# Kernel optimization log

Measured on AMD Instinct MI355X. Metric: run time of the kernel, lower is better.

Reference implementation:

```python
import jax, jax.numpy as jnp
import numpy as np
from itertools import product

B, D, H, W = 2, 32, 256, 256
N = 150000
C_IN, C_MID, C_OUT = 16, 32, 64
STRIDE, PAD, K = 2, 1, 3
DO = (D + 2 * PAD - K) // STRIDE + 1
HO = (H + 2 * PAD - K) // STRIDE + 1
WO = (W + 2 * PAD - K) // STRIDE + 1
EPS = 1e-5


def setup_inputs() -> dict:
    key = jax.random.key(0)
    ks = jax.random.split(key, 8)
    # unique active voxel coords via permutation of linear grid indices
    lin = jax.random.permutation(ks[0], B * D * H * W)[:N]
    b = lin // (D * H * W); r = lin % (D * H * W)
    z = r // (H * W); r = r % (H * W)
    y = r // W; x = r % W
    coords = jnp.stack([b, z, y, x], axis=1).astype(jnp.int32)  # [N,4] = (batch,z,y,x)
    feats = jax.random.normal(ks[1], (N, C_IN), jnp.float32)
    W1 = jax.random.normal(ks[2], (27, C_IN, C_MID), jnp.float32) * 0.08
    W2 = jax.random.normal(ks[3], (27, C_MID, C_MID), jnp.float32) * 0.06
    W3 = jax.random.normal(ks[4], (27, C_MID, C_OUT), jnp.float32) * 0.06
    b1 = jnp.zeros((C_MID,), jnp.float32); g1 = jnp.ones((C_MID,), jnp.float32); be1 = jnp.zeros((C_MID,), jnp.float32)
    b2 = jnp.zeros((C_MID,), jnp.float32); g2 = jnp.ones((C_MID,), jnp.float32); be2 = jnp.zeros((C_MID,), jnp.float32)
    b3 = jnp.zeros((C_OUT,), jnp.float32); g3 = jnp.ones((C_OUT,), jnp.float32); be3 = jnp.zeros((C_OUT,), jnp.float32)
    return dict(feats=feats, coords=coords, W1=W1, b1=b1, g1=g1, be1=be1,
                W2=W2, b2=b2, g2=g2, be2=be2, W3=W3, b3=b3, g3=g3, be3=be3)


def _bn_relu(x, g, b):
    # BatchNorm1d (training batch stats, biased var) over active voxels + ReLU
    m = x.mean(0)
    v = ((x - m) ** 2).mean(0)
    return jax.nn.relu((x - m) * jax.lax.rsqrt(v + EPS) * g + b)


def _subm_conv(feats, coords, grid, Wk, bias):
    # submanifold conv: gather neighbor features per kernel offset, GEMM, accumulate
    bb, zz, yy, xx = coords[:, 0], coords[:, 1], coords[:, 2], coords[:, 3]
    acc = jnp.zeros((feats.shape[0], Wk.shape[-1]), feats.dtype)
    for ki, (dz, dy, dx) in enumerate(product((-1, 0, 1), repeat=3)):
        nz, ny, nx = zz + dz, yy + dy, xx + dx
        valid = (nz >= 0) & (nz < D) & (ny >= 0) & (ny < H) & (nx >= 0) & (nx < W)
        lin = ((bb * D + jnp.clip(nz, 0, D - 1)) * H + jnp.clip(ny, 0, H - 1)) * W + jnp.clip(nx, 0, W - 1)
        nidx = jnp.where(valid, grid[lin], -1)
        gathered = jnp.where((nidx >= 0)[:, None], feats[jnp.maximum(nidx, 0)], 0.0)
        acc = acc + gathered @ Wk[ki]
    return acc + bias


def _sparse_down_conv(feats, coords, Wk, bias):
    # stride-2 SparseConv3d as GEMM + scatter-add into downsampled dense grid; mask = active outputs
    bb, zz, yy, xx = coords[:, 0], coords[:, 1], coords[:, 2], coords[:, 3]
    M = B * DO * HO * WO
    out = jnp.zeros((M, Wk.shape[-1]), feats.dtype)
    cnt = jnp.zeros((M,), jnp.int32)
    for ki, (kz, ky, kx) in enumerate(product(range(K), repeat=3)):
        oz, oy, ox = zz + PAD - kz, yy + PAD - ky, xx + PAD - kx
        valid = ((oz % STRIDE == 0) & (oy % STRIDE == 0) & (ox % STRIDE == 0) &
                 (oz >= 0) & (oy >= 0) & (ox >= 0) &
                 (oz // STRIDE < DO) & (oy // STRIDE < HO) & (ox // STRIDE < WO))
        lin = ((bb * DO + jnp.clip(oz // STRIDE, 0, DO - 1)) * HO
               + jnp.clip(oy // STRIDE, 0, HO - 1)) * WO + jnp.clip(ox // STRIDE, 0, WO - 1)
        lin = jnp.where(valid, lin, 0)
        contrib = jnp.where(valid[:, None], feats @ Wk[ki], 0.0)
        out = out.at[lin].add(contrib)
        cnt = cnt.at[lin].add(valid.astype(jnp.int32))
    mask = cnt > 0
    out = jnp.where(mask[:, None], out + bias, 0.0)
    return out, mask


def reference(feats, coords, W1, b1, g1, be1, W2, b2, g2, be2, W3, b3, g3, be3):
    lin0 = ((coords[:, 0] * D + coords[:, 1]) * H + coords[:, 2]) * W + coords[:, 3]
    grid = jnp.full((B * D * H * W,), -1, jnp.int32).at[lin0].set(jnp.arange(N, dtype=jnp.int32))
    x = _bn_relu(_subm_conv(feats, coords, grid, W1, b1), g1, be1)
    x = _bn_relu(_subm_conv(x, coords, grid, W2, b2), g2, be2)
    out, mask = _sparse_down_conv(x, coords, W3, b3)
    nact = jnp.maximum(mask.sum(), 1).astype(out.dtype)
    m = out.sum(0) / nact  # inactive rows are zero
    v = jnp.where(mask[:, None], (out - m) ** 2, 0.0).sum(0) / nact
    out = jax.nn.relu((out - m) * jax.lax.rsqrt(v + EPS) * g3 + be3)
    out = jnp.where(mask[:, None], out, 0.0)
    return out.reshape(B, DO, HO, WO, C_OUT)
```

## Files before the change

### kernel.cpp

```cpp
#include <hip/hip_runtime.h>

#define B_   2
#define D_   32
#define H_   256
#define W_   256
#define N_   150000
#define CIN  16
#define CMID 32
#define COUT 64
#define DO_  16
#define HO_  128
#define WO_  128
#define M_   (B_*DO_*HO_*WO_)
#define EPSf 1e-5f
#define NB_DOWN 8192
#define NREP 64

typedef _Float16 h2 __attribute__((ext_vector_type(2)));
__device__ inline h2 as_h2(unsigned u) { union { unsigned u; h2 h; } x; x.u = u; return x.h; }

#if defined(__has_builtin) && __has_builtin(__builtin_amdgcn_fdot2)
__device__ inline float dot2(unsigned f, unsigned w, float acc) {
    return __builtin_amdgcn_fdot2(as_h2(f), as_h2(w), acc, false);
}
#else
__device__ inline float dot2(unsigned f, unsigned w, float acc) {
    const h2 a = as_h2(f), b = as_h2(w);
    return fmaf((float)a.x, (float)b.x, fmaf((float)a.y, (float)b.y, acc));
}
#endif

__device__ inline unsigned hpk(float a, float b) {
    union { _Float16 h[2]; unsigned u; } x;
    x.h[0] = (_Float16)a; x.h[1] = (_Float16)b; return x.u;
}

__global__ __launch_bounds__(256) void k_scatter(const int* __restrict__ coords,
                                                 int* __restrict__ grid) {
    int i = blockIdx.x * 256 + threadIdx.x;
    if (i >= N_) return;
    const int4 c = *(const int4*)(coords + 4 * (size_t)i);
    grid[((c.x * D_ + c.y) * H_ + c.z) * W_ + c.w] = i;
}

__global__ __launch_bounds__(256) void k_twisth(const float* __restrict__ W1,
                                                const float* __restrict__ W2,
                                                const float* __restrict__ W3,
                                                uint4* __restrict__ Wh1,
                                                uint4* __restrict__ Wh2,
                                                uint4* __restrict__ Wh3) {
    const int t = blockIdx.x * 256 + threadIdx.x;
    if (t < 1728) {
        const int ki = t / 64, r = t % 64, half = r >> 5, sub = r & 31;
        const float* base = W1 + ki * 512 + (half * 8) * 32 + sub;
        uint4 o;
        o.x = hpk(base[0],   base[32]);
        o.y = hpk(base[64],  base[96]);
        o.z = hpk(base[128], base[160]);
        o.w = hpk(base[192], base[224]);
        Wh1[(ki * 2 + half) * 32 + sub] = o;
    } else if (t < 1728 + 3456) {
        const int u = t - 1728;
        const int ki = u / 128, r = u % 128, qh = r >> 5, sub = r & 31;
        const int half = qh >> 1, q = qh & 1;
        const float* base = W2 + ki * 1024 + (half * 16 + q * 8) * 32 + sub;
        uint4 o;
        o.x = hpk(base[0],   base[32]);
        o.y = hpk(base[64],  base[96]);
        o.z = hpk(base[128], base[160]);
        o.w = hpk(base[192], base[224]);
        Wh2[((ki * 2 + half) * 2 + q) * 32 + sub] = o;
    } else if (t < 1728 + 3456 + 6912) {
        const int u = t - 5184;
        const int ki = u / 256, r = u % 256, q = r >> 6, lane = r & 63;
        const float* base = W3 + ki * 2048 + (q * 8) * 64 + lane;
        uint4 o;
        o.x = hpk(base[0],   base[64]);
        o.y = hpk(base[128], base[192]);
        o.z = hpk(base[256], base[320]);
        o.w = hpk(base[384], base[448]);
        Wh3[(ki * 4 + q) * 64 + lane] = o;
    }
}

__global__ __launch_bounds__(256) void k_feat16(const float* __restrict__ F,
                                                unsigned* __restrict__ F16) {
    const int i = blockIdx.x * 256 + threadIdx.x;
    if (i >= N_ * CIN / 4) return;
    const float4 v = ((const float4*)F)[i];
    uint2 o; o.x = hpk(v.x, v.y); o.y = hpk(v.z, v.w);
    ((uint2*)F16)[i] = o;
}

template <int CI>
__global__ __launch_bounds__(256) void k_subm(const unsigned* __restrict__ X16,
                                              const int* __restrict__ coords,
                                              const int* __restrict__ grid,
                                              const uint4* __restrict__ Wh,
                                              const float* __restrict__ bias,
                                              _Float16* __restrict__ Yp,
                                              float* __restrict__ slab0) {
    constexpr int NQ = CI / 16;
    const int wid  = (blockIdx.x * 256 + threadIdx.x) >> 6;
    const int lane = threadIdx.x & 63;
    const int sub  = lane & 31;
    const int half = lane >> 5;
    const int i0   = wid * 4;

    int nidx01 = -1, nidx23 = -1;
    {
        const int4 cc = *(const int4*)(coords + 4 * (size_t)(i0 + half));
        if (sub < 27) {
            const int nz = cc.y + sub / 9 - 1;
            const int ny = cc.z + (sub / 3) % 3 - 1;
            const int nx = cc.w + sub % 3 - 1;
            if ((unsigned)nz < (unsigned)D_ && (unsigned)ny < (unsigned)H_ &&
                (unsigned)nx < (unsigned)W_)
                nidx01 = grid[((cc.x * D_ + nz) * H_ + ny) * W_ + nx];
        }
    }
    {
        const int4 cc = *(const int4*)(coords + 4 * (size_t)(i0 + 2 + half));
        if (sub < 27) {
            const int nz = cc.y + sub / 9 - 1;
            const int ny = cc.z + (sub / 3) % 3 - 1;
            const int nx = cc.w + sub % 3 - 1;
            if ((unsigned)nz < (unsigned)D_ && (unsigned)ny < (unsigned)H_ &&
                (unsigned)nx < (unsigned)W_)
                nidx23 = grid[((cc.x * D_ + nz) * H_ + ny) * W_ + nx];
        }
    }
    const unsigned long long a01 = __ballot(nidx01 >= 0);
    const unsigned long long a23 = __ballot(nidx23 >= 0);
    unsigned m0 = (unsigned)a01 & 0x7FFFFFFu;
    unsigned m1 = (unsigned)(a01 >> 32) & 0x7FFFFFFu;
    unsigned m2 = (unsigned)a23 & 0x7FFFFFFu;
    unsigned m3 = (unsigned)(a23 >> 32) & 0x7FFFFFFu;

    float acc0 = 0.f, acc1 = 0.f, acc2 = 0.f, acc3 = 0.f;

    auto tap = [&](int ki, int ni, float& acc) {
        const uint4* __restrict__ f =
            (const uint4*)(X16 + (size_t)ni * (CI / 2) + half * (CI / 4));
        const uint4* __restrict__ wb = Wh + ((size_t)(ki * 2 + half)) * NQ * 32 + sub;
#pragma unroll
        for (int q = 0; q < NQ; ++q) {
            const uint4 fu = f[q];
            const uint4 wu = wb[q * 32];
            acc = dot2(fu.x, wu.x, acc);
            acc = dot2(fu.y, wu.y, acc);
            acc = dot2(fu.z, wu.z, acc);
            acc = dot2(fu.w, wu.w, acc);
        }
    };

    while (m0 | m1 | m2 | m3) {
        if (m0) { const int ki = __builtin_ctz(m0); m0 &= m0 - 1;
                  tap(ki, __shfl(nidx01, ki, 64),      acc0); }
        if (m1) { const int ki = __builtin_ctz(m1); m1 &= m1 - 1;
                  tap(ki, __shfl(nidx01, ki + 32, 64), acc1); }
        if (m2) { const int ki = __builtin_ctz(m2); m2 &= m2 - 1;
                  tap(ki, __shfl(nidx23, ki, 64),      acc2); }
        if (m3) { const int ki = __builtin_ctz(m3); m3 &= m3 - 1;
                  tap(ki, __shfl(nidx23, ki + 32, 64), acc3); }
    }

    acc0 += __shfl_xor(acc0, 32, 64);
    acc1 += __shfl_xor(acc1, 32, 64);
    acc2 += __shfl_xor(acc2, 32, 64);
    acc3 += __shfl_xor(acc3, 32, 64);
    const float bv  = bias[sub];
    const float o01 = (half ? acc1 : acc0) + bv;
    const float o23 = (half ? acc3 : acc2) + bv;
    Yp[(size_t)(i0 + half) * 32 + sub]     = (_Float16)o01;
    Yp[(size_t)(i0 + 2 + half) * 32 + sub] = (_Float16)o23;

    __shared__ float sd[256];
    const int tid = threadIdx.x;
    float* __restrict__ slab = slab0 + (size_t)(blockIdx.x & (NREP - 1)) * 64;
    sd[tid] = o01 + o23;
    __syncthreads();
    if (tid < 32) {
        float t = 0.f;
#pragma unroll
        for (int k = 0; k < 8; ++k) t += sd[tid + 32 * k];
        atomicAdd(slab + tid, t);
    }
    __syncthreads();
    sd[tid] = o01 * o01 + o23 * o23;
    __syncthreads();
    if (tid < 32) {
        float t = 0.f;
#pragma unroll
        for (int k = 0; k < 8; ++k) t += sd[tid + 32 * k];
        atomicAdd(slab + 32 + tid, t);
    }
}

__global__ __launch_bounds__(256) void k_down(const unsigned* __restrict__ X16,
                                              const int* __restrict__ grid,
                                              const uint4* __restrict__ Wh3,
                                              const float* __restrict__ bias,
                                              _Float16* __restrict__ Yh,
                                              unsigned char* __restrict__ mask,
                                              float* __restrict__ slab0,
                                              int* __restrict__ nacts) {
    const int b    = blockIdx.x;
    const int swz  = (b & 7) * (NB_DOWN / 8) + (b >> 3);
    const int tid  = threadIdx.x;
    const int wv   = tid >> 6;
    const int lane = tid & 63;
    const int sub  = lane & 31;
    const int half = lane >> 5;

    const int vox0 = swz * 64;
    const int ox0  = vox0 & 127;
    int t = vox0 >> 7;
    const int oy = t & 127; t >>= 7;
    const int oz = t & 15;
    const int bb = t >> 4;

    __shared__ int   gl[9][132];
    __shared__ float sd[256];
    __shared__ int   scnt[4];

    const int gx0 = 2 * ox0 - 1;
    for (int e = tid; e < 9 * 132; e += 256) {
        const int r  = e / 132, xo = e % 132;
        const int z  = 2 * oz - 1 + r / 3;
        const int y  = 2 * oy - 1 + r % 3;
        const int x  = gx0 + xo;
        int v = -1;
        if ((unsigned)z < (unsigned)D_ && (unsigned)y < (unsigned)H_ &&
            (unsigned)x < (unsigned)W_ && xo < 129)
            v = grid[((bb * D_ + z) * H_ + y) * W_ + x];
        gl[r][xo] = v;
    }
    __syncthreads();

    const int dz = sub / 9, dy = (sub / 3) % 3, dx = sub % 3;
    const int row = (sub < 27) ? dz * 3 + dy : 0;

    const float bv = bias[lane];
    float s = 0.f, s2 = 0.f;
    int cnt = 0;

    auto tap = [&](int ki, int ni, float& acc) {
        const uint4* __restrict__ fS = (const uint4*)(X16 + (size_t)ni * 16);
        const uint4* __restrict__ wb = Wh3 + (size_t)ki * 256 + lane;
#pragma unroll
        for (int q = 0; q < 4; ++q) {
            const uint4 fu = fS[q];
            const uint4 wu = wb[q * 64];
            acc = dot2(fu.x, wu.x, acc);
            acc = dot2(fu.y, wu.y, acc);
            acc = dot2(fu.z, wu.z, acc);
            acc = dot2(fu.w, wu.w, acc);
        }
    };

    for (int it = 0; it < 4; ++it) {
        const int v0 = wv * 16 + it * 4;
        const int n01 = (sub < 27) ? gl[row][2 * (v0 + half) + dx] : -1;
        const int n23 = (sub < 27) ? gl[row][2 * (v0 + 2 + half) + dx] : -1;
        const unsigned long long a01 = __ballot(n01 >= 0);
        const unsigned long long a23 = __ballot(n23 >= 0);
        unsigned m0 = (unsigned)a01 & 0x7FFFFFFu;
        unsigned m1 = (unsigned)(a01 >> 32) & 0x7FFFFFFu;
        unsigned m2 = (unsigned)a23 & 0x7FFFFFFu;
        unsigned m3 = (unsigned)(a23 >> 32) & 0x7FFFFFFu;
        const int mk0 = m0 ? 1 : 0, mk1 = m1 ? 1 : 0;
        const int mk2 = m2 ? 1 : 0, mk3 = m3 ? 1 : 0;

        float ac0 = 0.f, ac1 = 0.f, ac2 = 0.f, ac3 = 0.f;
        while (m0 | m1 | m2 | m3) {
            if (m0) { const int ki = __builtin_ctz(m0); m0 &= m0 - 1;
                      tap(ki, __builtin_amdgcn_readfirstlane(__shfl(n01, ki, 64)),      ac0); }
            if (m1) { const int ki = __builtin_ctz(m1); m1 &= m1 - 1;
                      tap(ki, __builtin_amdgcn_readfirstlane(__shfl(n01, ki + 32, 64)), ac1); }
            if (m2) { const int ki = __builtin_ctz(m2); m2 &= m2 - 1;
                      tap(ki, __builtin_amdgcn_readfirstlane(__shfl(n23, ki, 64)),      ac2); }
            if (m3) { const int ki = __builtin_ctz(m3); m3 &= m3 - 1;
                      tap(ki, __builtin_amdgcn_readfirstlane(__shfl(n23, ki + 32, 64)), ac3); }
        }

        const int vg = vox0 + v0;
        const float o0 = mk0 ? ac0 + bv : 0.f;
        const float o1 = mk1 ? ac1 + bv : 0.f;
        const float o2 = mk2 ? ac2 + bv : 0.f;
        const float o3 = mk3 ? ac3 + bv : 0.f;
        Yh[(size_t)vg * COUT + lane]       = (_Float16)o0;
        Yh[(size_t)(vg + 1) * COUT + lane] = (_Float16)o1;
        Yh[(size_t)(vg + 2) * COUT + lane] = (_Float16)o2;
        Yh[(size_t)(vg + 3) * COUT + lane] = (_Float16)o3;
        if (lane == 0) {
            mask[vg]     = (unsigned char)mk0;
            mask[vg + 1] = (unsigned char)mk1;
            mask[vg + 2] = (unsigned char)mk2;
            mask[vg + 3] = (unsigned char)mk3;
            cnt += mk0 + mk1 + mk2 + mk3;
        }
        s  += o0 + o1 + o2 + o3;
        s2 += o0 * o0 + o1 * o1 + o2 * o2 + o3 * o3;
    }

    float* __restrict__ slab = slab0 + (size_t)(b & (NREP - 1)) * 128;
    sd[tid] = s;
    if (lane == 0) scnt[wv] = cnt;
    __syncthreads();
    if (tid < 64) atomicAdd(slab + tid, sd[tid] + sd[tid + 64] + sd[tid + 128] + sd[tid + 192]);
    __syncthreads();
    sd[tid] = s2;
    __syncthreads();
    if (tid < 64) atomicAdd(slab + 64 + tid, sd[tid] + sd[tid + 64] + sd[tid + 128] + sd[tid + 192]);
    if (tid == 0) atomicAdd(nacts + (b & (NREP - 1)), scnt[0] + scnt[1] + scnt[2] + scnt[3]);
}

template <int C>
__global__ void k_finslab(const float* __restrict__ slab0,
                          const float* __restrict__ g,
                          const float* __restrict__ be,
                          float n, float* __restrict__ ss) {
    const int c = threadIdx.x;
    if (c >= C) return;
    float sm = 0.f, s2 = 0.f;
    for (int r = 0; r < NREP; ++r) {
        sm += slab0[r * 2 * C + c];
        s2 += slab0[r * 2 * C + C + c];
    }
    const float m  = sm / n;
    const float v  = s2 / n - m * m;
    const float sc = g[c] * rsqrtf(v + EPSf);
    ss[c]     = sc;
    ss[C + c] = be[c] - m * sc;
}

__global__ void k_finstats3(const float* __restrict__ slab0,
                            const int* __restrict__ nacts,
                            const float* __restrict__ g,
                            const float* __restrict__ be,
                            float* __restrict__ ss) {
    const int c = threadIdx.x;
    if (c >= 64) return;
    float sm = 0.f, s2 = 0.f;
    int na = 0;
    for (int r = 0; r < NREP; ++r) {
        sm += slab0[r * 128 + c];
        s2 += slab0[r * 128 + 64 + c];
        na += nacts[r];
    }
    const float n  = (float)(na > 0 ? na : 1);
    const float m  = sm / n;
    const float v  = s2 / n - m * m;
    const float sc = g[c] * rsqrtf(v + EPSf);
    ss[c]      = sc;
    ss[64 + c] = be[c] - m * sc;
}

template <int C>
__global__ __launch_bounds__(256) void k_norm16(const unsigned* __restrict__ Yp2,
                                                const float* __restrict__ ss,
                                                unsigned* __restrict__ Xo16, long n4) {
    const long t = (long)blockIdx.x * 256 + threadIdx.x;
    if (t >= n4) return;
    const uint2 y = ((const uint2*)Yp2)[t];
    const h2 lo = as_h2(y.x), hi = as_h2(y.y);
    const int ch = (int)((t * 4) % C);
    float ox = fmaxf(fmaf((float)lo.x, ss[ch],     ss[C + ch]),     0.f);
    float oy = fmaxf(fmaf((float)lo.y, ss[ch + 1], ss[C + ch + 1]), 0.f);
    float oz = fmaxf(fmaf((float)hi.x, ss[ch + 2], ss[C + ch + 2]), 0.f);
    float ow = fmaxf(fmaf((float)hi.y, ss[ch + 3], ss[C + ch + 3]), 0.f);
    uint2 o; o.x = hpk(ox, oy); o.y = hpk(oz, ow);
    ((uint2*)Xo16)[t] = o;
}

__global__ __launch_bounds__(256) void k_norm3(const _Float16* __restrict__ Yh,
                                               const unsigned char* __restrict__ mask,
                                               const float* __restrict__ ss,
                                               float* __restrict__ out) {
    const long n4 = (long)M_ * COUT / 4;
    const long t = (long)blockIdx.x * 256 + threadIdx.x;
    if (t >= n4) return;
    const long vox = t >> 4;
    const int ch = (int)((t * 4) & 63);
    float4 o;
    if (mask[vox]) {
        const uint2 yu = *(const uint2*)(Yh + t * 4);
        const h2 ylo = as_h2(yu.x), yhi = as_h2(yu.y);
        o.x = fmaxf(fmaf((float)ylo.x, ss[ch],     ss[64 + ch]),     0.f);
        o.y = fmaxf(fmaf((float)ylo.y, ss[ch + 1], ss[64 + ch + 1]), 0.f);
        o.z = fmaxf(fmaf((float)yhi.x, ss[ch + 2], ss[64 + ch + 2]), 0.f);
        o.w = fmaxf(fmaf((float)yhi.y, ss[ch + 3], ss[64 + ch + 3]), 0.f);
    } else {
        o.x = o.y = o.z = o.w = 0.f;
    }
    ((float4*)out)[t] = o;
}

extern "C" void kernel_launch(void* const* d_in, const int* in_sizes, int n_in,
                              void* d_out, int out_size, void* d_ws, size_t ws_size,
                              hipStream_t stream) {
    const float* feats = (const float*)d_in[0];
    const int*   coords = (const int*)d_in[1];
    const float* W1 = (const float*)d_in[2];
    const float* b1 = (const float*)d_in[3];
    const float* g1 = (const float*)d_in[4];
    const float* be1 = (const float*)d_in[5];
    const float* W2 = (const float*)d_in[6];
    const float* b2 = (const float*)d_in[7];
    const float* g2 = (const float*)d_in[8];
    const float* be2 = (const float*)d_in[9];
    const float* W3 = (const float*)d_in[10];
    const float* b3 = (const float*)d_in[11];
    const float* g3 = (const float*)d_in[12];
    const float* be3 = (const float*)d_in[13];
    float* out = (float*)d_out;

    char* ws = (char*)d_ws;
    const size_t gridBytes = (size_t)B_ * D_ * H_ * W_ * 4;
    const size_t f16Bytes  = (size_t)N_ * CIN * 2;
    const size_t bufPBytes = (size_t)N_ * CMID * 2;
    const size_t YhBytes   = (size_t)M_ * COUT * 2;
    int*       grid   = (int*)ws;
    unsigned*  feat16 = (unsigned*)(ws + gridBytes);
    _Float16*  bufP   = (_Float16*)(ws + gridBytes + f16Bytes);
    unsigned*  bufH   = (unsigned*)(ws + gridBytes + f16Bytes + bufPBytes);
    _Float16*  Yh     = (_Float16*)(ws + gridBytes + f16Bytes + 2 * bufPBytes);
    unsigned char* mask = (unsigned char*)(ws + gridBytes + f16Bytes + 2 * bufPBytes + YhBytes);
    float* stats = (float*)(ws + gridBytes + f16Bytes + 2 * bufPBytes + YhBytes + (size_t)M_);

    float* ss1   = stats;
    float* ss2   = stats + 64;
    float* ss3   = stats + 128;
    float* slab1 = stats + 1024;
    float* slab2 = stats + 1024 + NREP * 64;
    float* slab3 = stats + 1024 + NREP * 128;
    int*   nacts = (int*)(stats + 1024 + NREP * 256);
    uint4* Wh1 = (uint4*)(stats + 32768);
    uint4* Wh2 = Wh1 + 1728;
    uint4* Wh3 = Wh2 + 3456;

    hipMemsetAsync(grid, 0xFF, gridBytes, stream);
    hipMemsetAsync(stats + 1024, 0, (NREP * 256 + NREP) * 4, stream);

    k_scatter<<<(N_ + 255) / 256, 256, 0, stream>>>(coords, grid);
    k_twisth<<<(12096 + 255) / 256, 256, 0, stream>>>(W1, W2, W3, Wh1, Wh2, Wh3);
    k_feat16<<<(N_ * CIN / 4 + 255) / 256, 256, 0, stream>>>(feats, feat16);

    const int nb_subm = N_ / 16;
    k_subm<CIN><<<nb_subm, 256, 0, stream>>>(feat16, coords, grid, Wh1, b1, bufP, slab1);
    k_finslab<CMID><<<1, 64, 0, stream>>>(slab1, g1, be1, (float)N_, ss1);
    k_norm16<CMID><<<(N_ * CMID / 4 + 255) / 256, 256, 0, stream>>>(
        (const unsigned*)bufP, ss1, bufH, (long)N_ * CMID / 4);

    k_subm<CMID><<<nb_subm, 256, 0, stream>>>(bufH, coords, grid, Wh2, b2, bufP, slab2);
    k_finslab<CMID><<<1, 64, 0, stream>>>(slab2, g2, be2, (float)N_, ss2);
    k_norm16<CMID><<<(N_ * CMID / 4 + 255) / 256, 256, 0, stream>>>(
        (const unsigned*)bufP, ss2, bufH, (long)N_ * CMID / 4);

    k_down<<<NB_DOWN, 256, 0, stream>>>(bufH, grid, Wh3, b3, Yh, mask, slab3, nacts);
    k_finstats3<<<1, 64, 0, stream>>>(slab3, nacts, g3, be3, ss3);
    k_norm3<<<(M_ * COUT / 4) / 256, 256, 0, stream>>>(Yh, mask, ss3, out);
}
```

Before: 239.7 us.

## Enlarge k_down tiles to two output rows and stage weights in LDS

The downsampling conv kernel now uses 1024-thread blocks, each covering 256 output voxels (two output rows) instead of 64. The grid halo is staged once per block for a 5x5 row window, so overlapping input rows are shared between the two output rows. All 27 tap weight matrices (about 110 KB) are copied into LDS and read from there rather than from global memory. The cost is a very large LDS footprint that limits occupancy to roughly one block per CU, plus the full weight load paid by every block, with fewer blocks in flight to hide gather latency.

```diff
diff --git a/kernel.cpp b/kernel.cpp
--- a/kernel.cpp
+++ b/kernel.cpp
@@ -13,7 +13,7 @@
 #define WO_  128
 #define M_   (B_*DO_*HO_*WO_)
 #define EPSf 1e-5f
-#define NB_DOWN 8192
+#define NB_DOWN 2048
 #define NREP 64
 
 typedef _Float16 h2 __attribute__((ext_vector_type(2)));
@@ -197,14 +197,14 @@
     }
 }
 
-__global__ __launch_bounds__(256) void k_down(const unsigned* __restrict__ X16,
-                                              const int* __restrict__ grid,
-                                              const uint4* __restrict__ Wh3,
-                                              const float* __restrict__ bias,
-                                              _Float16* __restrict__ Yh,
-                                              unsigned char* __restrict__ mask,
-                                              float* __restrict__ slab0,
-                                              int* __restrict__ nacts) {
+__global__ __launch_bounds__(1024) void k_down(const unsigned* __restrict__ X16,
+                                               const int* __restrict__ grid,
+                                               const uint4* __restrict__ Wh3,
+                                               const float* __restrict__ bias,
+                                               _Float16* __restrict__ Yh,
+                                               unsigned char* __restrict__ mask,
+                                               float* __restrict__ slab0,
+                                               int* __restrict__ nacts) {
     const int b    = blockIdx.x;
     const int swz  = (b & 7) * (NB_DOWN / 8) + (b >> 3);
     const int tid  = threadIdx.x;
@@ -213,33 +213,33 @@
     const int sub  = lane & 31;
     const int half = lane >> 5;
 
-    const int vox0 = swz * 64;
-    const int ox0  = vox0 & 127;
+    const int vox0 = swz * 256;
     int t = vox0 >> 7;
-    const int oy = t & 127; t >>= 7;
-    const int oz = t & 15;
-    const int bb = t >> 4;
-
-    __shared__ int   gl[9][132];
-    __shared__ float sd[256];
-    __shared__ int   scnt[4];
-
-    const int gx0 = 2 * ox0 - 1;
-    for (int e = tid; e < 9 * 132; e += 256) {
-        const int r  = e / 132, xo = e % 132;
-        const int z  = 2 * oz - 1 + r / 3;
-        const int y  = 2 * oy - 1 + r % 3;
-        const int x  = gx0 + xo;
+    const int oy0 = t & 127; t >>= 7;
+    const int oz  = t & 15;
+    const int bb  = t >> 4;
+
+    __shared__ uint4 lw[6912];
+    __shared__ int   lg[15 * 260];
+    __shared__ float sd[1024];
+    __shared__ int   scnt[16];
+
+    for (int e = tid; e < 6912; e += 1024) lw[e] = Wh3[e];
+    for (int e = tid; e < 15 * 260; e += 1024) {
+        const int r  = e / 260, xo = e % 260;
+        const int z  = 2 * oz  - 1 + r / 5;
+        const int y  = 2 * oy0 - 1 + r % 5;
+        const int x  = xo - 1;
         int v = -1;
         if ((unsigned)z < (unsigned)D_ && (unsigned)y < (unsigned)H_ &&
-            (unsigned)x < (unsigned)W_ && xo < 129)
+            (unsigned)x < (unsigned)W_ && xo < 258)
             v = grid[((bb * D_ + z) * H_ + y) * W_ + x];
-        gl[r][xo] = v;
+        lg[e] = v;
     }
     __syncthreads();
 
     const int dz = sub / 9, dy = (sub / 3) % 3, dx = sub % 3;
-    const int row = (sub < 27) ? dz * 3 + dy : 0;
+    const int rb = (sub < 27) ? (dz * 5 + dy) * 260 + dx : 0;
 
     const float bv = bias[lane];
     float s = 0.f, s2 = 0.f;
@@ -247,11 +247,10 @@
 
     auto tap = [&](int ki, int ni, float& acc) {
         const uint4* __restrict__ fS = (const uint4*)(X16 + (size_t)ni * 16);
-        const uint4* __restrict__ wb = Wh3 + (size_t)ki * 256 + lane;
 #pragma unroll
         for (int q = 0; q < 4; ++q) {
             const uint4 fu = fS[q];
-            const uint4 wu = wb[q * 64];
+            const uint4 wu = lw[ki * 256 + q * 64 + lane];
             acc = dot2(fu.x, wu.x, acc);
             acc = dot2(fu.y, wu.y, acc);
             acc = dot2(fu.z, wu.z, acc);
@@ -261,8 +260,13 @@
 
     for (int it = 0; it < 4; ++it) {
         const int v0 = wv * 16 + it * 4;
-        const int n01 = (sub < 27) ? gl[row][2 * (v0 + half) + dx] : -1;
-        const int n23 = (sub < 27) ? gl[row][2 * (v0 + 2 + half) + dx] : -1;
+        const int vA = v0 + half;
+        const int vB = v0 + 2 + half;
+        int n01 = -1, n23 = -1;
+        if (sub < 27) {
+            n01 = lg[rb + ((vA >> 7) * 2) * 260 + 2 * (vA & 127)];
+            n23 = lg[rb + ((vB >> 7) * 2) * 260 + 2 * (vB & 127)];
+        }
         const unsigned long long a01 = __ballot(n01 >= 0);
         const unsigned long long a23 = __ballot(n23 >= 0);
         unsigned m0 = (unsigned)a01 & 0x7FFFFFFu;
@@ -308,12 +312,27 @@
     sd[tid] = s;
     if (lane == 0) scnt[wv] = cnt;
     __syncthreads();
-    if (tid < 64) atomicAdd(slab + tid, sd[tid] + sd[tid + 64] + sd[tid + 128] + sd[tid + 192]);
+    if (tid < 64) {
+        float t2 = 0.f;
+#pragma unroll
+        for (int k = 0; k < 16; ++k) t2 += sd[tid + 64 * k];
+        atomicAdd(slab + tid, t2);
+    }
     __syncthreads();
     sd[tid] = s2;
     __syncthreads();
-    if (tid < 64) atomicAdd(slab + 64 + tid, sd[tid] + sd[tid + 64] + sd[tid + 128] + sd[tid + 192]);
-    if (tid == 0) atomicAdd(nacts + (b & (NREP - 1)), scnt[0] + scnt[1] + scnt[2] + scnt[3]);
+    if (tid < 64) {
+        float t2 = 0.f;
+#pragma unroll
+        for (int k = 0; k < 16; ++k) t2 += sd[tid + 64 * k];
+        atomicAdd(slab + 64 + tid, t2);
+    }
+    if (tid == 0) {
+        int c = 0;
+#pragma unroll
+        for (int k = 0; k < 16; ++k) c += scnt[k];
+        atomicAdd(nacts + (b & (NREP - 1)), c);
+    }
 }
 
 template <int C>
@@ -458,7 +477,7 @@
     k_norm16<CMID><<<(N_ * CMID / 4 + 255) / 256, 256, 0, stream>>>(
         (const unsigned*)bufP, ss2, bufH, (long)N_ * CMID / 4);
 
-    k_down<<<NB_DOWN, 256, 0, stream>>>(bufH, grid, Wh3, b3, Yh, mask, slab3, nacts);
+    k_down<<<NB_DOWN, 1024, 0, stream>>>(bufH, grid, Wh3, b3, Yh, mask, slab3, nacts);
     k_finstats3<<<1, 64, 0, stream>>>(slab3, nacts, g3, be3, ss3);
     k_norm3<<<(M_ * COUT / 4) / 256, 256, 0, stream>>>(Yh, mask, ss3, out);
 }
```

After: 258.9 us. +8.0%, slower.
